# Kernel optimization log

Hardware: AMD Instinct MI355X
Metric: run time of the kernel (lower is better)

## Reference

```python
import jax, jax.numpy as jnp
import numpy as np

NFE = 8            # round(time / step_size) = round(1.0 / 0.125)
STEP = 0.125


def setup_inputs() -> dict:
    key = jax.random.key(0)
    k1, k2, k3 = jax.random.split(key, 3)
    N, C, V, L = 64, 64, 500, 12
    x = jax.random.normal(k1, (N, C, V, L), dtype=jnp.float32)
    # random adjacency, row-normalized (typical diffusion operator; keeps Euler stable)
    adj = jax.random.uniform(k2, (V, V), dtype=jnp.float32)
    adj = adj / jnp.sum(adj, axis=1, keepdims=True)
    in_total = (NFE + 1) * C  # 576
    out_dim = 64
    W = jax.random.normal(k3, (out_dim, in_total), dtype=jnp.float32) * (1.0 / np.sqrt(in_total))
    b = jnp.zeros((out_dim,), dtype=jnp.float32)
    return {"x": x, "adj": adj, "W": W, "b": b}


def reference(x, adj, W, b):
    # Euler integration of dx/dt = A x over the node dim:
    # out[n,c,v,l] = sum_w x[n,c,w,l] * A[v,w]
    states = [x]
    cur = x
    for _ in range(NFE):  # fixed, small step count
        ax = jnp.einsum('ncwl,vw->ncvl', cur, adj)
        cur = cur + STEP * ax
        states.append(cur)
    h = jnp.concatenate(states, axis=1)  # [N, (NFE+1)*C, V, L]
    # 1x1 Conv2d == channel GEMM
    out = jnp.einsum('ncvl,oc->novl', h, W) + b[None, :, None, None]
    return out
```

## Files before the change

### kernel.cpp

```cpp
#include <hip/hip_runtime.h>
#include <hip/hip_bf16.h>
#include <stdint.h>

typedef __attribute__((ext_vector_type(8))) short short8;
typedef __attribute__((ext_vector_type(4))) short short4v;
typedef __attribute__((ext_vector_type(4))) float f32x4;
typedef __attribute__((ext_vector_type(4))) float fvec4;

__device__ __forceinline__ short f2bf(float f) {
  unsigned u = __builtin_bit_cast(unsigned, f);
  unsigned r = u + 0x7fffu + ((u >> 16) & 1u);
  return (short)(r >> 16);
}

__device__ __forceinline__ void gload_lds16(const void* g, void* l) {
  __builtin_amdgcn_global_load_lds(
      (const __attribute__((address_space(1))) void*)g,
      (__attribute__((address_space(3))) void*)l, 16, 0, 0);
}

#define VP   512
#define TILE_SHORTS 8192
#define PANEL_TILES 72
#define NSTEP 65

__device__ __forceinline__ int tswz(int r, int c) {
  return r * 64 + ((((c >> 3) ^ (r & 7)) << 3) | (c & 7));
}

__global__ __launch_bounds__(256) void initM_kernel(const float* __restrict__ adj,
    float* __restrict__ Mpow, short* __restrict__ Mt, short* __restrict__ M1T) {
  int idx = blockIdx.x * 256 + threadIdx.x;
  int v = idx >> 9, w = idx & 511;
  float m = 0.f;
  if (v < 500 && w < 500) m = 0.125f * adj[v * 500 + w] + (v == w ? 1.f : 0.f);
  Mpow[idx] = m;
  M1T[(size_t)w * VP + v] = f2bf(m);
  int bx = v >> 7, r = v & 127, c = w & 63;
  int kt0 = (w >> 6), kt1 = 8 + (w >> 6);
  Mt[(size_t)(bx * PANEL_TILES + kt0) * TILE_SHORTS + tswz(r, c)] =
      f2bf((v == w && v < 500) ? 1.f : 0.f);
  Mt[(size_t)(bx * PANEL_TILES + kt1) * TILE_SHORTS + tswz(r, c)] = f2bf(m);
}

__global__ __launch_bounds__(256) void powstep_kernel(const float* __restrict__ src,
    const short* __restrict__ M1T, float* __restrict__ dst,
    short* __restrict__ Mt, int kslice) {
  int tid = threadIdx.x, wv = tid >> 6, lane = tid & 63;
  int tile = blockIdx.x * 4 + wv;
  int tv = tile >> 5, tw = tile & 31;
  int row  = tv * 16 + (lane & 15);
  int colw = tw * 16 + (lane & 15);
  int kgrp = (lane >> 4) * 8;
  const short* mcol = M1T + (size_t)colw * VP;
  f32x4 acc = {0.f, 0.f, 0.f, 0.f};
  for (int k0 = 0; k0 < 512; k0 += 32) {
    int kc = k0 + kgrp;
    fvec4 f0 = *(const fvec4*)&src[row * VP + kc];
    fvec4 f1 = *(const fvec4*)&src[row * VP + kc + 4];
    short8 a;
    for (int t = 0; t < 4; ++t) { a[t] = f2bf(f0[t]); a[4 + t] = f2bf(f1[t]); }
    short8 b = *(const short8*)&mcol[kc];
    acc = __builtin_amdgcn_mfma_f32_16x16x32_bf16(a, b, acc, 0, 0, 0);
  }
  for (int r = 0; r < 4; ++r) {
    int i = (lane >> 4) * 4 + r;
    int vv = tv * 16 + i;
    float val = acc[r];
    dst[vv * VP + colw] = val;
    int bx = vv >> 7, rr = vv & 127, c = colw & 63;
    int kt = kslice * 8 + (colw >> 6);
    Mt[(size_t)(bx * PANEL_TILES + kt) * TILE_SHORTS + tswz(rr, c)] = f2bf(val);
  }
}

__global__ __launch_bounds__(256) void xpose_kernel(const float* __restrict__ x,
    short* __restrict__ xb) {
  int t = threadIdx.x, wv = t >> 6, lane = t & 63;
  int p  = blockIdx.x & 1;
  int w0 = (blockIdx.x >> 1) * 64;
  int n  = blockIdx.y;
  const float* xs = x + (size_t)n * 64 * 6000;
  __shared__ short xl[32 * 770];
  for (int ci = 0; ci < 8; ++ci) {
    int crow = wv * 8 + ci;
    int c = p * 32 + crow;
    for (int i = 0; i < 3; ++i) {
      int wl = (i * 64 + lane) * 4;
      int gwl = w0 * 12 + wl;
      fvec4 v = {0.f, 0.f, 0.f, 0.f};
      if (gwl + 3 < 6000) {
        v = *(const fvec4*)&xs[(size_t)c * 6000 + gwl];
      } else {
        for (int e = 0; e < 4; ++e)
          if (gwl + e < 6000) v[e] = xs[(size_t)c * 6000 + gwl + e];
      }
      for (int e = 0; e < 4; ++e) xl[crow * 770 + wl + e] = f2bf(v[e]);
    }
  }
  __syncthreads();
  for (int i = 0; i < 12; ++i) {
    int ct = i * 256 + t;
    int bl = ct & 3;
    int w_l = (ct >> 2) & 63;
    int l = ct >> 8;
    short8 s;
    for (int j = 0; j < 8; ++j)
      s[j] = xl[(bl * 8 + j) * 770 + w_l * 12 + l];
    size_t dst = ((size_t)(n * 12 + l) * 512 + w0 + w_l) * 64 + (p * 4 + bl) * 8;
    *(short8*)(xb + dst) = s;
  }
}

__global__ __launch_bounds__(256) void zbuild_kernel(const short* __restrict__ xb,
    const float* __restrict__ W, short* __restrict__ Zt, int n0) {
  int t = threadIdx.x, wv = t >> 6, lane = t & 63;
  int lh = blockIdx.x;
  int l = lh >> 1, wh = lh & 1;
  int nloc = blockIdx.y;
  int n = n0 + nloc;
  const short* xbase = xb + (size_t)(n * 12 + l) * 512 * 64;
  short8 af[4][2];
  for (int q = 0; q < 4; ++q)
    for (int ks = 0; ks < 2; ++ks) {
      int wrow = wh * 256 + wv * 64 + q * 16 + (lane & 15);
      int cblk = ks * 4 + (lane >> 4);
      af[q][ks] = *(const short8*)(xbase + (size_t)wrow * 64 + cblk * 8);
    }
  int lanebase = (lane & 15) * 12 + l;
  int kt_off = wh * 4 + wv;
  for (int j = 0; j < 36; ++j) {
    int k = j >> 2;
    int o = (j & 3) * 16 + (lane & 15);
    const float* wp = W + o * 576 + k * 64;
    short8 bw[2];
    for (int ks = 0; ks < 2; ++ks) {
      fvec4 f0 = *(const fvec4*)(wp + ks * 32 + (lane >> 4) * 8);
      fvec4 f1 = *(const fvec4*)(wp + ks * 32 + (lane >> 4) * 8 + 4);
      for (int e = 0; e < 4; ++e) { bw[ks][e] = f2bf(f0[e]); bw[ks][4 + e] = f2bf(f1[e]); }
    }
    f32x4 acc[4];
    for (int q = 0; q < 4; ++q) {
      acc[q] = (f32x4){0.f, 0.f, 0.f, 0.f};
      acc[q] = __builtin_amdgcn_mfma_f32_16x16x32_bf16(af[q][0], bw[0], acc[q], 0, 0, 0);
      acc[q] = __builtin_amdgcn_mfma_f32_16x16x32_bf16(af[q][1], bw[1], acc[q], 0, 0, 0);
    }
    int zr = (j & 3) * 192 + lanebase;
    int pr = zr >> 7, rr = zr & 127;
    size_t tbase = ((size_t)(nloc * 6 + pr) * PANEL_TILES + k * 8 + kt_off) * TILE_SHORTS
                 + rr * 64;
    for (int q = 0; q < 4; ++q) {
      int c4 = q * 16 + (lane >> 4) * 4;
      size_t idx = tbase + ((((c4 >> 3) ^ (zr & 7)) << 3) | (c4 & 7));
      short4v s;
      for (int e = 0; e < 4; ++e) s[e] = f2bf(acc[q][e]);
      *(short4v*)(Zt + idx) = s;
    }
  }
}

__global__ __launch_bounds__(256) void biggemm_kernel(const short* __restrict__ Zt,
    const short* __restrict__ Mt, const float* __restrict__ bvec,
    float* __restrict__ out, int n0) {
  int tid = threadIdx.x, wv = tid >> 6, lane = tid & 63;
  int nwg = gridDim.x;
  int b = blockIdx.x;
  int swz = (b & 7) * (nwg >> 3) + (b >> 3);
  int bx = swz & 7;
  int rest = swz >> 3;
  int by = rest % 6;
  int bz = rest / 6;
  int v0    = bx * 64;
  int rowM0 = by * 128;
  int n = n0 + bz;
  __shared__ short As[2][TILE_SHORTS];
  __shared__ short Bs[2][TILE_SHORTS / 2];
  f32x4 acc[2][4];
  for (int i = 0; i < 2; ++i)
    for (int j = 0; j < 4; ++j) acc[i][j] = (f32x4){0.f, 0.f, 0.f, 0.f};
  const char* Apanel = (const char*)(Zt + (size_t)(bz * 6 + by) * PANEL_TILES * TILE_SHORTS);
  const char* Bpanel = (const char*)(Mt + (size_t)(bx >> 1) * PANEL_TILES * TILE_SHORTS)
                     + (bx & 1) * 8192;

  auto ktmap = [&](int s) { return (s == 0) ? bx : (s + 7); };

  auto STAGE = [&](int p, int kt) {
    const char* a  = Apanel + (size_t)kt * (TILE_SHORTS * 2);
    const char* bb = Bpanel + (size_t)kt * (TILE_SHORTS * 2);
#pragma unroll
    for (int cc = 0; cc < 4; ++cc) {
      int chunk = cc * 4 + wv;
      int off = chunk * 1024 + lane * 16;
      gload_lds16(a + off, (char*)As[p] + chunk * 1024);
    }
#pragma unroll
    for (int cc = 0; cc < 2; ++cc) {
      int chunk = cc * 4 + wv;
      int off = chunk * 1024 + lane * 16;
      gload_lds16(bb + off, (char*)Bs[p] + chunk * 1024);
    }
  };

  STAGE(0, ktmap(0));
  STAGE(1, ktmap(1));

  for (int s = 0; s < NSTEP; ++s) {
    int d = s & 1;
    if (s < NSTEP - 1) {
      asm volatile("s_waitcnt vmcnt(6)" ::: "memory");
    } else {
      asm volatile("s_waitcnt vmcnt(0)" ::: "memory");
    }
    __builtin_amdgcn_sched_barrier(0);
    __builtin_amdgcn_s_barrier();

    short8 af[2][2], bf[2][4];
#pragma unroll
    for (int kk = 0; kk < 2; ++kk) {
      int cbyte = kk * 64 + (lane >> 4) * 16;
#pragma unroll
      for (int mi = 0; mi < 2; ++mi) {
        int r = wv * 32 + mi * 16 + (lane & 15);
        af[kk][mi] = *(const short8*)((const char*)As[d] + r * 128 + (cbyte ^ ((r & 7) << 4)));
      }
#pragma unroll
      for (int ni = 0; ni < 4; ++ni) {
        int r2 = ni * 16 + (lane & 15);
        bf[kk][ni] = *(const short8*)((const char*)Bs[d] + r2 * 128 + (cbyte ^ ((r2 & 7) << 4)));
      }
    }
    asm volatile("s_waitcnt lgkmcnt(0)" ::: "memory");
    __builtin_amdgcn_sched_barrier(0);
    __builtin_amdgcn_s_barrier();

    if (s + 2 < NSTEP) STAGE(d, ktmap(s + 2));

    __builtin_amdgcn_s_setprio(1);
#pragma unroll
    for (int kk = 0; kk < 2; ++kk)
#pragma unroll
      for (int mi = 0; mi < 2; ++mi)
#pragma unroll
        for (int ni = 0; ni < 4; ++ni)
          acc[mi][ni] = __builtin_amdgcn_mfma_f32_16x16x32_bf16(af[kk][mi], bf[kk][ni],
                                                                acc[mi][ni], 0, 0, 0);
    __builtin_amdgcn_s_setprio(0);
  }

  for (int mi = 0; mi < 2; ++mi) {
    for (int r = 0; r < 4; ++r) {
      int gm = rowM0 + wv * 32 + mi * 16 + (lane >> 4) * 4 + r;
      int o = gm / 12, l = gm - o * 12;
      float bo = bvec[o];
      size_t obase = (((size_t)n * 64 + o) * 500) * 12 + l;
      for (int ni = 0; ni < 4; ++ni) {
        int v = v0 + ni * 16 + (lane & 15);
        if (v < 500) out[obase + (size_t)v * 12] = acc[mi][ni][r] + bo;
      }
    }
  }
}

extern "C" void kernel_launch(void* const* d_in, const int* in_sizes, int n_in,
                              void* d_out, int out_size, void* d_ws, size_t ws_size,
                              hipStream_t stream) {
  const float* x   = (const float*)d_in[0];
  const float* adj = (const float*)d_in[1];
  const float* W   = (const float*)d_in[2];
  const float* bv  = (const float*)d_in[3];
  float* out = (float*)d_out;
  char* ws = (char*)d_ws;

  size_t off = 0;
  float* Mpow0 = (float*)(ws + off); off += (size_t)512 * 512 * 4;
  float* Mpow1 = (float*)(ws + off); off += (size_t)512 * 512 * 4;
  short* M1T   = (short*)(ws + off); off += (size_t)512 * 512 * 2;
  short* Mt    = (short*)(ws + off); off += (size_t)4 * PANEL_TILES * TILE_SHORTS * 2;
  short* xb    = (short*)(ws + off); off += (size_t)64 * 12 * 512 * 64 * 2;
  short* Zt    = (short*)(ws + off);
  size_t per_n = (size_t)6 * PANEL_TILES * TILE_SHORTS * 2;
  int nchunk = 1;
  if (ws_size > off) {
    size_t a = (ws_size - off) / per_n;
    nchunk = (a >= 16) ? 16 : (a < 1 ? 1 : (int)a);
  }

  hipLaunchKernelGGL(initM_kernel, dim3(1024), dim3(256), 0, stream, adj, Mpow0, Mt, M1T);
  const float* src = Mpow0; float* dst = Mpow1;
  for (int k = 2; k <= 8; ++k) {
    hipLaunchKernelGGL(powstep_kernel, dim3(256), dim3(256), 0, stream, src, M1T, dst, Mt, k);
    float* t = dst; dst = (float*)src; src = t;
  }
  hipLaunchKernelGGL(xpose_kernel, dim3(16, 64), dim3(256), 0, stream, x, xb);
  for (int n0 = 0; n0 < 64; n0 += nchunk) {
    int cn = (64 - n0) < nchunk ? (64 - n0) : nchunk;
    hipLaunchKernelGGL(zbuild_kernel, dim3(24, cn), dim3(256), 0, stream, xb, W, Zt, n0);
    hipLaunchKernelGGL(biggemm_kernel, dim3(48 * cn), dim3(256), 0, stream, Zt, Mt, bv, out, n0);
  }
}
```

Before: 589.1 us.

## Split K across wave pairs in biggemm with LDS reduction epilogue

Changes the biggemm wave layout from four waves each owning 32 rows over the full K tile to a 2x2 arrangement. Each wave now covers 64 rows on one half of the K tile, so B-fragment LDS reads drop per MFMA. The partial sums are combined through an LDS reduction buffer after the main loop. The cost is twice the accumulator registers per wave and an extra synchronized reduction before the output writes.

```diff
diff --git a/kernel.cpp b/kernel.cpp
--- a/kernel.cpp
+++ b/kernel.cpp
@@ -173,10 +173,12 @@
   int v0    = bx * 64;
   int rowM0 = by * 128;
   int n = n0 + bz;
-  __shared__ short As[2][TILE_SHORTS];
-  __shared__ short Bs[2][TILE_SHORTS / 2];
-  f32x4 acc[2][4];
-  for (int i = 0; i < 2; ++i)
+  int wr = wv & 1, wk = wv >> 1;
+  __shared__ short lds[3 * TILE_SHORTS];
+  short* Asp0 = lds;
+  short* Bsp0 = lds + 2 * TILE_SHORTS;
+  f32x4 acc[4][4];
+  for (int i = 0; i < 4; ++i)
     for (int j = 0; j < 4; ++j) acc[i][j] = (f32x4){0.f, 0.f, 0.f, 0.f};
   const char* Apanel = (const char*)(Zt + (size_t)(bz * 6 + by) * PANEL_TILES * TILE_SHORTS);
   const char* Bpanel = (const char*)(Mt + (size_t)(bx >> 1) * PANEL_TILES * TILE_SHORTS)
@@ -187,22 +189,26 @@
   auto STAGE = [&](int p, int kt) {
     const char* a  = Apanel + (size_t)kt * (TILE_SHORTS * 2);
     const char* bb = Bpanel + (size_t)kt * (TILE_SHORTS * 2);
+    char* asd = (char*)(Asp0 + p * TILE_SHORTS);
+    char* bsd = (char*)(Bsp0 + p * (TILE_SHORTS / 2));
 #pragma unroll
     for (int cc = 0; cc < 4; ++cc) {
       int chunk = cc * 4 + wv;
       int off = chunk * 1024 + lane * 16;
-      gload_lds16(a + off, (char*)As[p] + chunk * 1024);
+      gload_lds16(a + off, asd + chunk * 1024);
     }
 #pragma unroll
     for (int cc = 0; cc < 2; ++cc) {
       int chunk = cc * 4 + wv;
       int off = chunk * 1024 + lane * 16;
-      gload_lds16(bb + off, (char*)Bs[p] + chunk * 1024);
+      gload_lds16(bb + off, bsd + chunk * 1024);
     }
   };
 
   STAGE(0, ktmap(0));
   STAGE(1, ktmap(1));
+
+  int cbyte = wk * 64 + (lane >> 4) * 16;
 
   for (int s = 0; s < NSTEP; ++s) {
     int d = s & 1;
@@ -214,20 +220,18 @@
     __builtin_amdgcn_sched_barrier(0);
     __builtin_amdgcn_s_barrier();
 
-    short8 af[2][2], bf[2][4];
-#pragma unroll
-    for (int kk = 0; kk < 2; ++kk) {
-      int cbyte = kk * 64 + (lane >> 4) * 16;
-#pragma unroll
-      for (int mi = 0; mi < 2; ++mi) {
-        int r = wv * 32 + mi * 16 + (lane & 15);
-        af[kk][mi] = *(const short8*)((const char*)As[d] + r * 128 + (cbyte ^ ((r & 7) << 4)));
-      }
-#pragma unroll
-      for (int ni = 0; ni < 4; ++ni) {
-        int r2 = ni * 16 + (lane & 15);
-        bf[kk][ni] = *(const short8*)((const char*)Bs[d] + r2 * 128 + (cbyte ^ ((r2 & 7) << 4)));
-      }
+    const char* asd = (const char*)(Asp0 + d * TILE_SHORTS);
+    const char* bsd = (const char*)(Bsp0 + d * (TILE_SHORTS / 2));
+    short8 af[4], bf[4];
+#pragma unroll
+    for (int mi = 0; mi < 4; ++mi) {
+      int r = wr * 64 + mi * 16 + (lane & 15);
+      af[mi] = *(const short8*)(asd + r * 128 + (cbyte ^ ((r & 7) << 4)));
+    }
+#pragma unroll
+    for (int ni = 0; ni < 4; ++ni) {
+      int r2 = ni * 16 + (lane & 15);
+      bf[ni] = *(const short8*)(bsd + r2 * 128 + (cbyte ^ ((r2 & 7) << 4)));
     }
     asm volatile("s_waitcnt lgkmcnt(0)" ::: "memory");
     __builtin_amdgcn_sched_barrier(0);
@@ -237,25 +241,42 @@
 
     __builtin_amdgcn_s_setprio(1);
 #pragma unroll
-    for (int kk = 0; kk < 2; ++kk)
-#pragma unroll
-      for (int mi = 0; mi < 2; ++mi)
+    for (int mi = 0; mi < 4; ++mi)
+#pragma unroll
+      for (int ni = 0; ni < 4; ++ni)
+        acc[mi][ni] = __builtin_amdgcn_mfma_f32_16x16x32_bf16(af[mi], bf[ni],
+                                                              acc[mi][ni], 0, 0, 0);
+    __builtin_amdgcn_s_setprio(0);
+  }
+
+  float* red = (float*)lds;
+  __syncthreads();
+  if (wk) {
+#pragma unroll
+    for (int mi = 0; mi < 4; ++mi)
+#pragma unroll
+      for (int r = 0; r < 4; ++r) {
+        int row = wr * 64 + mi * 16 + (lane >> 4) * 4 + r;
 #pragma unroll
         for (int ni = 0; ni < 4; ++ni)
-          acc[mi][ni] = __builtin_amdgcn_mfma_f32_16x16x32_bf16(af[kk][mi], bf[kk][ni],
-                                                                acc[mi][ni], 0, 0, 0);
-    __builtin_amdgcn_s_setprio(0);
-  }
-
-  for (int mi = 0; mi < 2; ++mi) {
-    for (int r = 0; r < 4; ++r) {
-      int gm = rowM0 + wv * 32 + mi * 16 + (lane >> 4) * 4 + r;
-      int o = gm / 12, l = gm - o * 12;
-      float bo = bvec[o];
-      size_t obase = (((size_t)n * 64 + o) * 500) * 12 + l;
-      for (int ni = 0; ni < 4; ++ni) {
-        int v = v0 + ni * 16 + (lane & 15);
-        if (v < 500) out[obase + (size_t)v * 12] = acc[mi][ni][r] + bo;
+          red[row * 65 + ni * 16 + (lane & 15)] = acc[mi][ni][r];
+      }
+  }
+  __syncthreads();
+  if (!wk) {
+    for (int mi = 0; mi < 4; ++mi) {
+      for (int r = 0; r < 4; ++r) {
+        int row = wr * 64 + mi * 16 + (lane >> 4) * 4 + r;
+        int gm = rowM0 + row;
+        int o = gm / 12, l = gm - o * 12;
+        float bo = bvec[o];
+        size_t obase = (((size_t)n * 64 + o) * 500) * 12 + l;
+        for (int ni = 0; ni < 4; ++ni) {
+          int v = v0 + ni * 16 + (lane & 15);
+          if (v < 500)
+            out[obase + (size_t)v * 12] =
+                acc[mi][ni][r] + red[row * 65 + ni * 16 + (lane & 15)] + bo;
+        }
       }
     }
   }
```

Result: no change. 586.0 us (-0.5%).
